# Optimization experiments

Hardware: AMD Instinct MI355X
Metric: run time of the kernel (lower is better)

The kernel has to match this reference:

```python
import jax, jax.numpy as jnp
import numpy as np

COMMITMENT_COST = 0.25
NUM_EMBEDDINGS = 8192
EMBEDDING_DIM = 256


def setup_inputs() -> dict:
    key = jax.random.key(0)
    k1, k2 = jax.random.split(key)
    inputs = jax.random.normal(k1, (32, 256, EMBEDDING_DIM), dtype=jnp.float32)
    codebook = jax.random.normal(k2, (NUM_EMBEDDINGS, EMBEDDING_DIM), dtype=jnp.float32)
    # match nn.Embedding init: N(0,1) then L2-normalize rows
    codebook = codebook / jnp.linalg.norm(codebook, axis=1, keepdims=True)
    return {"inputs": inputs, "codebook": codebook}


def reference(inputs, codebook):
    B, K, D = inputs.shape
    flat = inputs.reshape(-1, D).astype(jnp.float32)  # [N, D], N = B*K
    N = flat.shape[0]

    distances = (
        jnp.sum(flat * flat, axis=1, keepdims=True)
        + jnp.sum(codebook * codebook, axis=1)
        - 2.0 * flat @ codebook.T
    )
    indices = jnp.argmin(distances, axis=1)  # [N]

    # codebook lookup (equivalent to one-hot @ codebook)
    quantized = codebook[indices].reshape(B, K, D)

    e_latent_loss = jnp.mean((jax.lax.stop_gradient(quantized) - inputs) ** 2)
    q_latent_loss = jnp.mean((quantized - jax.lax.stop_gradient(inputs)) ** 2)
    loss = q_latent_loss + COMMITMENT_COST * e_latent_loss

    # straight-through estimator
    quantized_ste = inputs + jax.lax.stop_gradient(quantized - inputs)

    # perplexity from codebook usage histogram (== mean of one-hot encodings)
    counts = jnp.zeros((NUM_EMBEDDINGS,), dtype=jnp.float32).at[indices].add(1.0)
    avg_probs = counts / N
    perplexity = jnp.exp(-jnp.sum(avg_probs * jnp.log(avg_probs + 1e-10)))

    return quantized_ste, loss, perplexity
```

## Files before the change

kernel.cpp:

```cpp
#include <hip/hip_runtime.h>
#include <math.h>

#define NTOK 8192
#define NEMB 8192
#define DIM  256
#define NPB  64

typedef _Float16 f16x8 __attribute__((ext_vector_type(8)));
typedef _Float16 f16x4 __attribute__((ext_vector_type(4)));
typedef float    f32x4 __attribute__((ext_vector_type(4)));

__global__ __launch_bounds__(256) void convert_kernel(
        const float* __restrict__ X, const float* __restrict__ C,
        _Float16* __restrict__ Xh, _Float16* __restrict__ Ch,
        float* __restrict__ cnorm, int* __restrict__ counts) {
    const bool isC = (blockIdx.y != 0);
    if (isC && blockIdx.x < 8) {
        ((int4*)counts)[blockIdx.x * 256 + threadIdx.x] = make_int4(0, 0, 0, 0);
    }
    const float* src = isC ? C : X;
    _Float16* dst = isC ? Ch : Xh;
    size_t t = (size_t)blockIdx.x * 256 + threadIdx.x;
    float4 x = *(const float4*)&src[t * 4];
    f16x4 h;
    h[0] = (_Float16)x.x; h[1] = (_Float16)x.y;
    h[2] = (_Float16)x.z; h[3] = (_Float16)x.w;
    *(f16x4*)&dst[t * 4] = h;
    if (isC) {
        float s = x.x * x.x + x.y * x.y + x.z * x.z + x.w * x.w;
        #pragma unroll
        for (int off = 32; off >= 1; off >>= 1) s += __shfl_xor(s, off);
        if ((threadIdx.x & 63) == 0) cnorm[t >> 6] = s;
    }
}

__device__ __forceinline__ void stage_pair(
        const _Float16* __restrict__ Ag, const _Float16* __restrict__ Bg,
        _Float16* Abase, _Float16* Bbase, int t) {
    #pragma unroll
    for (int c = 0; c < 4; ++c) {
        int gr  = c * 256 + t;
        int row = gr >> 3;
        int kg  = (gr & 7) ^ (row & 7);
        __builtin_amdgcn_global_load_lds(
            (const __attribute__((address_space(1))) void*)(Ag + (size_t)row * DIM + kg * 8),
            (__attribute__((address_space(3))) void*)(Abase + (size_t)gr * 8), 16, 0, 0);
        __builtin_amdgcn_global_load_lds(
            (const __attribute__((address_space(1))) void*)(Bg + (size_t)row * DIM + kg * 8),
            (__attribute__((address_space(3))) void*)(Bbase + (size_t)gr * 8), 16, 0, 0);
    }
}

__device__ __forceinline__ void compute_pair(
        const _Float16* Abase, const _Float16* Bbase,
        f32x4 (&acc)[4][4], int wm, int wn, int lrow, int g) {
    #pragma unroll
    for (int ks = 0; ks < 2; ++ks) {
        const int kg = ks * 4 + g;
        f16x8 af[4], bf_[4];
        #pragma unroll
        for (int tm = 0; tm < 4; ++tm) {
            int row = wm + tm * 16 + lrow;
            af[tm] = *(const f16x8*)&Abase[(row * 8 + (kg ^ (row & 7))) * 8];
        }
        #pragma unroll
        for (int tn = 0; tn < 4; ++tn) {
            int row = wn + tn * 16 + lrow;
            bf_[tn] = *(const f16x8*)&Bbase[(row * 8 + (kg ^ (row & 7))) * 8];
        }
        #pragma unroll
        for (int tm = 0; tm < 4; ++tm)
            #pragma unroll
            for (int tn = 0; tn < 4; ++tn)
                acc[tm][tn] = __builtin_amdgcn_mfma_f32_16x16x32_f16(
                    af[tm], bf_[tn], acc[tm][tn], 0, 0, 0);
    }
}

__global__ __launch_bounds__(256) void mfma_argmin_kernel(
        const _Float16* __restrict__ Xh, const _Float16* __restrict__ Ch,
        const float* __restrict__ cnorm,
        float* __restrict__ minv_p, int* __restrict__ mini_p) {
    __shared__ __align__(16) _Float16 lds[32768];

    const int t = threadIdx.x;
    const int wid = t >> 6, lane = t & 63;
    const int tb0 = blockIdx.x * 128;
    const int cb0 = blockIdx.y * 128;
    const int wm = (wid >> 1) * 64;
    const int wn = (wid & 1) * 64;
    const int lrow = lane & 15;
    const int g = lane >> 4;

    f32x4 acc[4][4];
    #pragma unroll
    for (int a = 0; a < 4; ++a)
        #pragma unroll
        for (int b = 0; b < 4; ++b) acc[a][b] = (f32x4)0.0f;

    const _Float16* Ag = Ch + (size_t)cb0 * DIM;
    const _Float16* Bg = Xh + (size_t)tb0 * DIM;

    stage_pair(Ag, Bg, lds, lds + 8192, t);
    __syncthreads();
    #pragma unroll
    for (int p = 0; p < 4; ++p) {
        _Float16* cur = lds + (p & 1) * 16384;
        if (p < 3) {
            _Float16* nxt = lds + ((p + 1) & 1) * 16384;
            stage_pair(Ag + (p + 1) * 64, Bg + (p + 1) * 64, nxt, nxt + 8192, t);
        }
        compute_pair(cur, cur + 8192, acc, wm, wn, lrow, g);
        __syncthreads();
    }

    float* cn_lds = (float*)lds;
    float* cmb_v  = (float*)lds + 128;
    int*   cmb_i  = (int*)((float*)lds + 384);
    if (t < 128) cn_lds[t] = cnorm[cb0 + t];
    __syncthreads();

    float cn[16];
    #pragma unroll
    for (int tm = 0; tm < 4; ++tm)
        #pragma unroll
        for (int reg = 0; reg < 4; ++reg)
            cn[tm * 4 + reg] = cn_lds[wm + tm * 16 + g * 4 + reg];

    #pragma unroll
    for (int tn = 0; tn < 4; ++tn) {
        float bv = 1e30f; int bi = 0x7fffffff;
        #pragma unroll
        for (int tm = 0; tm < 4; ++tm) {
            #pragma unroll
            for (int reg = 0; reg < 4; ++reg) {
                float d = fmaf(-2.0f, acc[tm][tn][reg], cn[tm * 4 + reg]);
                int code = cb0 + wm + tm * 16 + g * 4 + reg;
                if (d < bv) { bv = d; bi = code; }
            }
        }
        #pragma unroll
        for (int off = 16; off <= 32; off <<= 1) {
            float ov = __shfl_xor(bv, off);
            int   oi = __shfl_xor(bi, off);
            if (ov < bv || (ov == bv && oi < bi)) { bv = ov; bi = oi; }
        }
        if (g == 0) {
            int tl = wn + tn * 16 + lrow;
            cmb_v[tl * 2 + (wid >> 1)] = bv;
            cmb_i[tl * 2 + (wid >> 1)] = bi;
        }
    }
    __syncthreads();
    if (t < 128) {
        float v0 = cmb_v[t * 2], v1 = cmb_v[t * 2 + 1];
        int   i0 = cmb_i[t * 2], i1 = cmb_i[t * 2 + 1];
        bool tk = (v1 < v0) || (v1 == v0 && i1 < i0);
        minv_p[(size_t)blockIdx.y * NTOK + tb0 + t] = tk ? v1 : v0;
        mini_p[(size_t)blockIdx.y * NTOK + tb0 + t] = tk ? i1 : i0;
    }
}

__global__ __launch_bounds__(256) void reduce_gather_kernel(
        const float* __restrict__ X, const float* __restrict__ C,
        const float* __restrict__ minv_p, const int* __restrict__ mini_p,
        int* __restrict__ counts, float* __restrict__ out,
        float* __restrict__ psum) {
    __shared__ int   idx_lds[32];
    __shared__ float wsum[4];
    const int m0 = blockIdx.x * 32;
    const int t = threadIdx.x;
    {
        const int tl = t >> 3;
        const int pc = t & 7;
        int token = m0 + tl;
        float bv = 1e30f; int bi = 0x7fffffff;
        #pragma unroll
        for (int i = 0; i < 8; ++i) {
            int p = pc * 8 + i;
            float v  = minv_p[(size_t)p * NTOK + token];
            int   ii = mini_p[(size_t)p * NTOK + token];
            if (v < bv || (v == bv && ii < bi)) { bv = v; bi = ii; }
        }
        #pragma unroll
        for (int off = 1; off < 8; off <<= 1) {
            float ov = __shfl_xor(bv, off);
            int   oi = __shfl_xor(bi, off);
            if (ov < bv || (ov == bv && oi < bi)) { bv = ov; bi = oi; }
        }
        if (pc == 0) { idx_lds[tl] = bi; atomicAdd(&counts[bi], 1); }
    }
    __syncthreads();
    const int wid = t >> 6, lane = t & 63;
    float local = 0.0f;
    #pragma unroll
    for (int r = 0; r < 8; ++r) {
        int token = m0 + wid * 8 + r;
        int e = idx_lds[wid * 8 + r];
        float4 q = *(const float4*)&C[(size_t)e * DIM + lane * 4];
        float4 x = *(const float4*)&X[(size_t)token * DIM + lane * 4];
        *(float4*)&out[(size_t)token * DIM + lane * 4] = q;
        float d0 = q.x - x.x, d1 = q.y - x.y, d2 = q.z - x.z, d3 = q.w - x.w;
        local += d0 * d0 + d1 * d1 + d2 * d2 + d3 * d3;
    }
    #pragma unroll
    for (int off = 32; off >= 1; off >>= 1) local += __shfl_xor(local, off);
    if (lane == 0) wsum[wid] = local;
    __syncthreads();
    if (t == 0) psum[blockIdx.x] = wsum[0] + wsum[1] + wsum[2] + wsum[3];
}

__global__ __launch_bounds__(256) void finalize_kernel(
        const int* __restrict__ counts, const float* __restrict__ psum,
        float* __restrict__ out) {
    const int t = threadIdx.x;
    double local = 0.0;
    #pragma unroll 1
    for (int e = t; e < NEMB; e += 256) {
        float p = (float)counts[e] * (1.0f / (float)NTOK);
        local += (double)(p * logf(p + 1e-10f));
    }
    float ls = psum[t];
    #pragma unroll
    for (int off = 32; off >= 1; off >>= 1) {
        local += __shfl_xor(local, off);
        ls    += __shfl_xor(ls, off);
    }
    __shared__ double she[4];
    __shared__ float  shs[4];
    int lane = t & 63, wid = t >> 6;
    if (lane == 0) { she[wid] = local; shs[wid] = ls; }
    __syncthreads();
    if (t == 0) {
        double ent = she[0] + she[1] + she[2] + she[3];
        float  ssq = shs[0] + shs[1] + shs[2] + shs[3];
        out[(size_t)NTOK * DIM]     = 1.25f * ssq / (float)((size_t)NTOK * DIM);
        out[(size_t)NTOK * DIM + 1] = expf((float)(-ent));
    }
}

extern "C" void kernel_launch(void* const* d_in, const int* in_sizes, int n_in,
                              void* d_out, int out_size, void* d_ws, size_t ws_size,
                              hipStream_t stream) {
    const float* X = (const float*)d_in[0];
    const float* C = (const float*)d_in[1];
    float* out = (float*)d_out;

    char* ws = (char*)d_ws;
    size_t o = 0;
    _Float16* Xh = (_Float16*)(ws + o); o += (size_t)NTOK * DIM * 2;
    _Float16* Ch = (_Float16*)(ws + o); o += (size_t)NEMB * DIM * 2;
    float* cnorm  = (float*)(ws + o); o += (size_t)NEMB * 4;
    float* minv_p = (float*)(ws + o); o += (size_t)NPB * NTOK * 4;
    int*   mini_p = (int*)  (ws + o); o += (size_t)NPB * NTOK * 4;
    int*   counts = (int*)  (ws + o); o += (size_t)NEMB * 4;
    float* psum   = (float*)(ws + o);

    convert_kernel<<<dim3(NTOK * DIM / 4 / 256, 2), 256, 0, stream>>>(
        X, C, Xh, Ch, cnorm, counts);
    mfma_argmin_kernel<<<dim3(NTOK / 128, NEMB / 128), 256, 0, stream>>>(
        Xh, Ch, cnorm, minv_p, mini_p);
    reduce_gather_kernel<<<256, 256, 0, stream>>>(
        X, C, minv_p, mini_p, counts, out, psum);
    finalize_kernel<<<1, 256, 0, stream>>>(counts, psum, out);
}
```

Before: 135.7 us.

## Reduce argmin partials with 64-bit atomicMin and fuse finalize into gather kernel

Each argmin block now packs its per-token minimum distance (offset so it stays positive) and index into a 64-bit key and does an atomicMin, replacing the 64-way partial arrays and their cross-block reduction. The loss is computed from the stored distance plus a precomputed per-token norm instead of rereading X. The finalize step is folded into the gather kernel with a last-block-done counter, which removes one launch. The trade-offs are atomic contention, float-precision loss from reconstructing the squared error through the distance identity, and reliance on the positive-offset ordering trick.

```diff
diff --git a/kernel.cpp b/kernel.cpp
--- a/kernel.cpp
+++ b/kernel.cpp
@@ -4,7 +4,6 @@
 #define NTOK 8192
 #define NEMB 8192
 #define DIM  256
-#define NPB  64
 
 typedef _Float16 f16x8 __attribute__((ext_vector_type(8)));
 typedef _Float16 f16x4 __attribute__((ext_vector_type(4)));
@@ -13,10 +12,20 @@
 __global__ __launch_bounds__(256) void convert_kernel(
         const float* __restrict__ X, const float* __restrict__ C,
         _Float16* __restrict__ Xh, _Float16* __restrict__ Ch,
-        float* __restrict__ cnorm, int* __restrict__ counts) {
+        float* __restrict__ cnorm, float* __restrict__ xnorm,
+        unsigned long long* __restrict__ keys, int* __restrict__ aux_zero) {
     const bool isC = (blockIdx.y != 0);
     if (isC && blockIdx.x < 8) {
-        ((int4*)counts)[blockIdx.x * 256 + threadIdx.x] = make_int4(0, 0, 0, 0);
+        ((int4*)aux_zero)[blockIdx.x * 256 + threadIdx.x] = make_int4(0, 0, 0, 0);
+        if (blockIdx.x == 0 && threadIdx.x == 0) {
+            aux_zero[8192] = 0;
+            ((float*)aux_zero)[8193] = 0.0f;
+        }
+    }
+    if (!isC && blockIdx.x < 8) {
+        int4 ff = make_int4(-1, -1, -1, -1);
+        ((int4*)keys)[blockIdx.x * 512 + threadIdx.x * 2]     = ff;
+        ((int4*)keys)[blockIdx.x * 512 + threadIdx.x * 2 + 1] = ff;
     }
     const float* src = isC ? C : X;
     _Float16* dst = isC ? Ch : Xh;
@@ -26,11 +35,11 @@
     h[0] = (_Float16)x.x; h[1] = (_Float16)x.y;
     h[2] = (_Float16)x.z; h[3] = (_Float16)x.w;
     *(f16x4*)&dst[t * 4] = h;
-    if (isC) {
-        float s = x.x * x.x + x.y * x.y + x.z * x.z + x.w * x.w;
-        #pragma unroll
-        for (int off = 32; off >= 1; off >>= 1) s += __shfl_xor(s, off);
-        if ((threadIdx.x & 63) == 0) cnorm[t >> 6] = s;
+    float s = x.x * x.x + x.y * x.y + x.z * x.z + x.w * x.w;
+    #pragma unroll
+    for (int off = 32; off >= 1; off >>= 1) s += __shfl_xor(s, off);
+    if ((threadIdx.x & 63) == 0) {
+        if (isC) cnorm[t >> 6] = s; else xnorm[t >> 6] = s;
     }
 }
 
@@ -80,7 +89,7 @@
 __global__ __launch_bounds__(256) void mfma_argmin_kernel(
         const _Float16* __restrict__ Xh, const _Float16* __restrict__ Ch,
         const float* __restrict__ cnorm,
-        float* __restrict__ minv_p, int* __restrict__ mini_p) {
+        unsigned long long* __restrict__ keys) {
     __shared__ __align__(16) _Float16 lds[32768];
 
     const int t = threadIdx.x;
@@ -156,86 +165,68 @@
         float v0 = cmb_v[t * 2], v1 = cmb_v[t * 2 + 1];
         int   i0 = cmb_i[t * 2], i1 = cmb_i[t * 2 + 1];
         bool tk = (v1 < v0) || (v1 == v0 && i1 < i0);
-        minv_p[(size_t)blockIdx.y * NTOK + tb0 + t] = tk ? v1 : v0;
-        mini_p[(size_t)blockIdx.y * NTOK + tb0 + t] = tk ? i1 : i0;
-    }
-}
-
-__global__ __launch_bounds__(256) void reduce_gather_kernel(
-        const float* __restrict__ X, const float* __restrict__ C,
-        const float* __restrict__ minv_p, const int* __restrict__ mini_p,
-        int* __restrict__ counts, float* __restrict__ out,
-        float* __restrict__ psum) {
+        float bv = tk ? v1 : v0;
+        int   bi = tk ? i1 : i0;
+        unsigned long long key =
+            ((unsigned long long)__builtin_bit_cast(unsigned, bv + 64.0f) << 32)
+            | (unsigned)bi;
+        atomicMin(&keys[tb0 + t], key);
+    }
+}
+
+__global__ __launch_bounds__(256) void gather_finalize_kernel(
+        const float* __restrict__ C, const unsigned long long* __restrict__ keys,
+        const float* __restrict__ xnorm, int* __restrict__ counts,
+        float* __restrict__ out) {
     __shared__ int   idx_lds[32];
-    __shared__ float wsum[4];
+    __shared__ int   last_flag;
+    int* done    = counts + NEMB;
+    float* lossp = (float*)(counts + NEMB + 1);
     const int m0 = blockIdx.x * 32;
     const int t = threadIdx.x;
-    {
-        const int tl = t >> 3;
-        const int pc = t & 7;
-        int token = m0 + tl;
-        float bv = 1e30f; int bi = 0x7fffffff;
-        #pragma unroll
-        for (int i = 0; i < 8; ++i) {
-            int p = pc * 8 + i;
-            float v  = minv_p[(size_t)p * NTOK + token];
-            int   ii = mini_p[(size_t)p * NTOK + token];
-            if (v < bv || (v == bv && ii < bi)) { bv = v; bi = ii; }
-        }
-        #pragma unroll
-        for (int off = 1; off < 8; off <<= 1) {
-            float ov = __shfl_xor(bv, off);
-            int   oi = __shfl_xor(bi, off);
-            if (ov < bv || (ov == bv && oi < bi)) { bv = ov; bi = oi; }
-        }
-        if (pc == 0) { idx_lds[tl] = bi; atomicAdd(&counts[bi], 1); }
+    if (t < 32) {
+        unsigned long long k = keys[m0 + t];
+        int bi  = (int)(unsigned)k;
+        float d = __builtin_bit_cast(float, (unsigned)(k >> 32)) - 64.0f;
+        idx_lds[t] = bi;
+        atomicAdd(&counts[bi], 1);
+        float lt = d + xnorm[m0 + t];
+        #pragma unroll
+        for (int off = 1; off < 32; off <<= 1) lt += __shfl_xor(lt, off);
+        if (t == 0) atomicAdd(lossp, lt);
     }
     __syncthreads();
     const int wid = t >> 6, lane = t & 63;
-    float local = 0.0f;
     #pragma unroll
     for (int r = 0; r < 8; ++r) {
         int token = m0 + wid * 8 + r;
         int e = idx_lds[wid * 8 + r];
         float4 q = *(const float4*)&C[(size_t)e * DIM + lane * 4];
-        float4 x = *(const float4*)&X[(size_t)token * DIM + lane * 4];
         *(float4*)&out[(size_t)token * DIM + lane * 4] = q;
-        float d0 = q.x - x.x, d1 = q.y - x.y, d2 = q.z - x.z, d3 = q.w - x.w;
-        local += d0 * d0 + d1 * d1 + d2 * d2 + d3 * d3;
-    }
-    #pragma unroll
-    for (int off = 32; off >= 1; off >>= 1) local += __shfl_xor(local, off);
-    if (lane == 0) wsum[wid] = local;
-    __syncthreads();
-    if (t == 0) psum[blockIdx.x] = wsum[0] + wsum[1] + wsum[2] + wsum[3];
-}
-
-__global__ __launch_bounds__(256) void finalize_kernel(
-        const int* __restrict__ counts, const float* __restrict__ psum,
-        float* __restrict__ out) {
-    const int t = threadIdx.x;
-    double local = 0.0;
-    #pragma unroll 1
-    for (int e = t; e < NEMB; e += 256) {
-        float p = (float)counts[e] * (1.0f / (float)NTOK);
-        local += (double)(p * logf(p + 1e-10f));
-    }
-    float ls = psum[t];
-    #pragma unroll
-    for (int off = 32; off >= 1; off >>= 1) {
-        local += __shfl_xor(local, off);
-        ls    += __shfl_xor(ls, off);
-    }
-    __shared__ double she[4];
-    __shared__ float  shs[4];
-    int lane = t & 63, wid = t >> 6;
-    if (lane == 0) { she[wid] = local; shs[wid] = ls; }
-    __syncthreads();
-    if (t == 0) {
-        double ent = she[0] + she[1] + she[2] + she[3];
-        float  ssq = shs[0] + shs[1] + shs[2] + shs[3];
-        out[(size_t)NTOK * DIM]     = 1.25f * ssq / (float)((size_t)NTOK * DIM);
-        out[(size_t)NTOK * DIM + 1] = expf((float)(-ent));
+    }
+    __threadfence();
+    if (t == 0) last_flag = (atomicAdd(done, 1) == 255);
+    __syncthreads();
+    if (last_flag) {
+        double local = 0.0;
+        #pragma unroll 1
+        for (int e = t; e < NEMB; e += 256) {
+            int c = atomicAdd(&counts[e], 0);
+            float p = (float)c * (1.0f / (float)NTOK);
+            local += (double)(p * logf(p + 1e-10f));
+        }
+        #pragma unroll
+        for (int off = 32; off >= 1; off >>= 1) local += __shfl_xor(local, off);
+        __shared__ double she[4];
+        int lane2 = t & 63, wid2 = t >> 6;
+        if (lane2 == 0) she[wid2] = local;
+        __syncthreads();
+        if (t == 0) {
+            double ent = she[0] + she[1] + she[2] + she[3];
+            float ssq = atomicAdd(lossp, 0.0f);
+            out[(size_t)NTOK * DIM]     = 1.25f * ssq / (float)((size_t)NTOK * DIM);
+            out[(size_t)NTOK * DIM + 1] = expf((float)(-ent));
+        }
     }
 }
 
@@ -250,17 +241,15 @@
     size_t o = 0;
     _Float16* Xh = (_Float16*)(ws + o); o += (size_t)NTOK * DIM * 2;
     _Float16* Ch = (_Float16*)(ws + o); o += (size_t)NEMB * DIM * 2;
-    float* cnorm  = (float*)(ws + o); o += (size_t)NEMB * 4;
-    float* minv_p = (float*)(ws + o); o += (size_t)NPB * NTOK * 4;
-    int*   mini_p = (int*)  (ws + o); o += (size_t)NPB * NTOK * 4;
-    int*   counts = (int*)  (ws + o); o += (size_t)NEMB * 4;
-    float* psum   = (float*)(ws + o);
+    float* cnorm = (float*)(ws + o); o += (size_t)NEMB * 4;
+    float* xnorm = (float*)(ws + o); o += (size_t)NTOK * 4;
+    unsigned long long* keys = (unsigned long long*)(ws + o); o += (size_t)NTOK * 8;
+    int* counts  = (int*)(ws + o);   o += (size_t)(NEMB + 4) * 4;
 
     convert_kernel<<<dim3(NTOK * DIM / 4 / 256, 2), 256, 0, stream>>>(
-        X, C, Xh, Ch, cnorm, counts);
+        X, C, Xh, Ch, cnorm, xnorm, keys, counts);
     mfma_argmin_kernel<<<dim3(NTOK / 128, NEMB / 128), 256, 0, stream>>>(
-        Xh, Ch, cnorm, minv_p, mini_p);
-    reduce_gather_kernel<<<256, 256, 0, stream>>>(
-        X, C, minv_p, mini_p, counts, out, psum);
-    finalize_kernel<<<1, 256, 0, stream>>>(counts, psum, out);
-}
+        Xh, Ch, cnorm, keys);
+    gather_finalize_kernel<<<256, 256, 0, stream>>>(
+        C, keys, xnorm, counts, out);
+}
```

Result: slower. 162.9 us (+20.1%).
